# Kernel tuning notes

Hardware: AMD Instinct MI355X
Metric: run time of the kernel (lower is better)

## Reference

```python
import jax, jax.numpy as jnp
import numpy as np

B, NNODES, C = 8192, 6, 256

def _compute_W(features, W_id):
    # features: [B, C', N] -> edge weights [B, N, N, 2] (J2 operator: [I, exp-affinity - 10*I])
    f = jnp.swapaxes(features, 1, 2)                        # [B, N, C']
    sq = jnp.sum(f * f, axis=2, keepdims=True)              # [B, N, 1]
    D = jax.nn.relu(sq + jnp.swapaxes(sq, 1, 2)
                    - 2.0 * jnp.einsum('bnc,bmc->bnm', f, f))   # pairwise sq-dist [B,N,N]
    D_std = jnp.std(D, axis=(1, 2), ddof=1, keepdims=True)  # unbiased, matches torch.std
    D = jnp.exp(-2.0 * D / D_std)
    W_new = D[..., None] - 10.0 * W_id                      # 'softmax' branch is a no-op reshape in source
    return jnp.concatenate([W_id, W_new], axis=3)

def setup_inputs() -> dict:
    key = jax.random.key(0)
    ks = jax.random.split(key, 3)
    x = jax.random.normal(ks[0], (B, NNODES, C), dtype=jnp.float32)
    K1Nopen = jax.random.normal(ks[1], (C, C), dtype=jnp.float32) * 0.1
    KNclose = jax.random.normal(ks[2], (NNODES, C), dtype=jnp.float32) * 0.1
    alpha = jnp.zeros((1, 1), dtype=jnp.float32)
    h = jnp.array([0.1], dtype=jnp.float32)
    return {"x": x, "K1Nopen": K1Nopen, "KNclose": KNclose, "alpha": alpha, "h": h}

def reference(x, K1Nopen, KNclose, alpha, h):
    Bq, N, _ = x.shape
    W_id = jnp.broadcast_to(jnp.eye(N, dtype=x.dtype)[None, :, :, None], (Bq, N, N, 1))
    xn = jnp.swapaxes(x, 1, 2)                                  # [B, C, N]
    xn = jax.nn.relu(jnp.einsum('oc,bcn->bon', K1Nopen, xn))    # singleLayer (1x1 conv + relu); dropout = identity
    xn_old = xn
    beta = jax.nn.sigmoid(alpha)
    al = (1.0 - beta) / h
    be = beta / (h * h)
    for _ in range(4):
        Wi = _compute_W(xn, W_id)
        W1 = Wi[..., 1]                                         # [B, N, N]
        g = W1[:, None] * (xn[:, :, None, :] - xn[:, :, :, None])  # nodeGrad [B,C,N,N]
        d = g
        for _t in range(5):                                     # finalDoubleLayer: edgeConv no-ops on 4-D input
            d = jnp.tanh(d)
        dxn = jnp.sum(W1[:, None] * d, axis=2)                  # edgeDiv -> [B, C, N]
        xn, xn_old = (2.0 * be * xn - be * xn_old + al * xn - dxn) / (be + al), xn
    out = jnp.swapaxes(jnp.einsum('oc,bcn->bon', KNclose, xn), 1, 2)  # [B, N, NNODES]
    Wl = _compute_W(out, W_id)
    return out[:, 0, :], xn, Wl
```

## Files before the change

kernel.cpp:

```cpp
#include <hip/hip_runtime.h>
#include <math.h>

#define NNODES 6
#define CDIM 256
#define NPAIR 15
#define BTOT 8192

#define XN_OFF   49152ULL
#define WL_OFF   12632064ULL

typedef __attribute__((ext_vector_type(8))) short short8v;
typedef __attribute__((ext_vector_type(4))) float f32x4;

static __device__ __forceinline__ unsigned bf16_rne(float f) {
  unsigned u = __float_as_uint(f);
  return (u + 0x7FFFu + ((u >> 16) & 1u)) >> 16;
}

static __device__ __forceinline__ float tanh1(float v) {
  float e = __expf(2.0f * v);
  return 1.0f - __fdividef(2.0f, e + 1.0f);
}

template <int CTRL>
static __device__ __forceinline__ float dpp_add(float v) {
  int s = __builtin_bit_cast(int, v);
  int t = __builtin_amdgcn_update_dpp(s, s, CTRL, 0xF, 0xF, false);
  return v + __builtin_bit_cast(float, t);
}
static __device__ __forceinline__ float wave_sum(float v) {
  v = dpp_add<0xB1>(v);
  v = dpp_add<0x4E>(v);
  v = dpp_add<0x141>(v);
  v = dpp_add<0x140>(v);
  int s = __builtin_bit_cast(int, v);
  int t = __builtin_amdgcn_ds_swizzle(s, 0x401F);
  v += __builtin_bit_cast(float, t);
  v += __shfl_xor(v, 32, 64);
  return v;
}

__global__ void split_k1(const float* __restrict__ K1,
                         uint4* __restrict__ Ah, uint4* __restrict__ Al) {
  int t = blockIdx.x * 256 + threadIdx.x;
  int o = t >> 5, c8 = t & 31;
  const float* src = K1 + (size_t)o * 256 + c8 * 8;
  unsigned hi[8], lo[8];
#pragma unroll
  for (int j = 0; j < 8; ++j) {
    float f = src[j];
    unsigned hr = bf16_rne(f);
    float hf = __uint_as_float(hr << 16);
    lo[j] = bf16_rne(f - hf);
    hi[j] = hr;
  }
  int s = c8 >> 2, ko = c8 & 3, mt = o >> 4, row = o & 15;
  int idx16 = ((s * 16 + mt) * 4 + ko) * 16 + row;
  Ah[idx16] = make_uint4(hi[0] | (hi[1] << 16), hi[2] | (hi[3] << 16),
                         hi[4] | (hi[5] << 16), hi[6] | (hi[7] << 16));
  Al[idx16] = make_uint4(lo[0] | (lo[1] << 16), lo[2] | (lo[3] << 16),
                         lo[4] | (lo[5] << 16), lo[6] | (lo[7] << 16));
}

__global__ __launch_bounds__(256, 2) void pdegcn_mfma(
    const float* __restrict__ x,
    const uint4* __restrict__ Ahg,
    const uint4* __restrict__ Alg,
    const float* __restrict__ KNc,
    const float* __restrict__ alphap,
    const float* __restrict__ hp,
    float* __restrict__ out)
{
  __shared__ unsigned short bbuf[14528];
  __shared__ float Tt[1024];
  __shared__ float Ms[4][36];

  const int wv = threadIdx.x >> 6;
  const int lane = threadIdx.x & 63;
  const int b0 = blockIdx.x * 4;

#pragma unroll
  for (int t = 0; t < 4; ++t) {
    int i = threadIdx.x + 256 * t;
    float v = ((float)(i - 512) + 0.5f) * (1.0f / 64.0f);
#pragma unroll
    for (int r = 0; r < 5; ++r) v = tanh1(v);
    Tt[i] = v;
  }

  {
    const float4* x4 = reinterpret_cast<const float4*>(x) + (size_t)b0 * 384;
#pragma unroll
    for (int i = 0; i < 6; ++i) {
      int idx = threadIdx.x + 256 * i;
      int p = idx >> 6, c4 = idx & 63;
      float4 v = x4[idx];
      unsigned w0 = __builtin_amdgcn_perm(__float_as_uint(v.y), __float_as_uint(v.x), 0x07060302u);
      unsigned w1 = __builtin_amdgcn_perm(__float_as_uint(v.w), __float_as_uint(v.z), 0x07060302u);
      int ko = c4 >> 1, jb = (c4 & 1) * 4;
      int colS = p ^ (ko & 7);
      int hw = (ko * 24 + colS) * 8 + jb;
      *reinterpret_cast<uint2*>(&bbuf[hw]) = make_uint2(w0, w1);
    }
  }
  __syncthreads();

  f32x4 acc[4][2];
#pragma unroll
  for (int m = 0; m < 4; ++m)
#pragma unroll
    for (int nt = 0; nt < 2; ++nt)
      acc[m][nt] = (f32x4){0.0f, 0.0f, 0.0f, 0.0f};

  const int g = lane >> 4, colx = lane & 15;
  const short8v* Ah8 = reinterpret_cast<const short8v*>(Ahg);
  const short8v* Al8 = reinterpret_cast<const short8v*>(Alg);
  const short8v* bb16 = reinterpret_cast<const short8v*>(bbuf);

#pragma unroll 2
  for (int s = 0; s < 8; ++s) {
    int ko = s * 4 + g;
    int q = ko & 7;
    short8v bh[2];
#pragma unroll
    for (int nt = 0; nt < 2; ++nt) {
      int off16 = ko * 24 + ((nt * 16 + colx) ^ q);
      bh[nt] = bb16[off16];
    }
#pragma unroll
    for (int m = 0; m < 4; ++m) {
      int mt = wv * 4 + m;
      int ai = (s * 16 + mt) * 64 + lane;
      short8v a_h = Ah8[ai];
      short8v a_l = Al8[ai];
#pragma unroll
      for (int nt = 0; nt < 2; ++nt) {
        acc[m][nt] = __builtin_amdgcn_mfma_f32_16x16x32_bf16(a_h, bh[nt], acc[m][nt], 0, 0, 0);
        acc[m][nt] = __builtin_amdgcn_mfma_f32_16x16x32_bf16(a_l, bh[nt], acc[m][nt], 0, 0, 0);
      }
    }
  }
  __syncthreads();

  float* xn_lds = reinterpret_cast<float*>(bbuf);
#pragma unroll
  for (int m = 0; m < 4; ++m) {
    int mt = wv * 4 + m;
#pragma unroll
    for (int nt = 0; nt < 2; ++nt) {
      int bn = nt * 16 + colx;
      if (bn < 24) {
        f32x4 v = acc[m][nt];
        float4 w4 = make_float4(fmaxf(v[0], 0.0f), fmaxf(v[1], 0.0f),
                                fmaxf(v[2], 0.0f), fmaxf(v[3], 0.0f));
        int cidx = (mt * 16 + g * 4) ^ ((bn & 7) << 2);
        *reinterpret_cast<float4*>(&xn_lds[bn * 256 + cidx]) = w4;
      }
    }
  }
  __syncthreads();

  const int c0 = lane * 4;
  float xn[4][6], xo[4][6];
#pragma unroll
  for (int n = 0; n < 6; ++n) {
    int row = wv * 6 + n;
    float4 t = *reinterpret_cast<const float4*>(&xn_lds[row * 256 + (c0 ^ ((row & 7) << 2))]);
    xn[0][n] = t.x; xn[1][n] = t.y; xn[2][n] = t.z; xn[3][n] = t.w;
    xo[0][n] = t.x; xo[1][n] = t.y; xo[2][n] = t.z; xo[3][n] = t.w;
  }
  __syncthreads();

  {
    uint4* kh4 = reinterpret_cast<uint4*>(reinterpret_cast<char*>(bbuf) + 12672);
    uint4* kl4 = kh4 + 512;
#pragma unroll
    for (int cc = 0; cc < 2; ++cc) {
      int c = threadIdx.x + cc * 256;
      int row = c & 15, ko = (c >> 4) & 3, s = c >> 6;
      uint4 hi4 = make_uint4(0, 0, 0, 0), lo4 = make_uint4(0, 0, 0, 0);
      if (row < 6) {
        const float4* src = reinterpret_cast<const float4*>(KNc + row * 256 + s * 32 + ko * 8);
        float4 f0 = src[0], f1 = src[1];
        float f[8] = {f0.x, f0.y, f0.z, f0.w, f1.x, f1.y, f1.z, f1.w};
        unsigned hh[8], ll[8];
#pragma unroll
        for (int j = 0; j < 8; ++j) {
          unsigned hr = bf16_rne(f[j]);
          float hf = __uint_as_float(hr << 16);
          ll[j] = bf16_rne(f[j] - hf);
          hh[j] = hr;
        }
        hi4 = make_uint4(hh[0] | (hh[1] << 16), hh[2] | (hh[3] << 16),
                         hh[4] | (hh[5] << 16), hh[6] | (hh[7] << 16));
        lo4 = make_uint4(ll[0] | (ll[1] << 16), ll[2] | (ll[3] << 16),
                         ll[4] | (ll[5] << 16), ll[6] | (ll[7] << 16));
      }
      kh4[c] = hi4;
      kl4[c] = lo4;
    }
  }
  __syncthreads();

  const float alpha = alphap[0];
  const float h = hp[0];
  const float beta = 1.0f / (1.0f + __expf(-alpha));
  const float al = (1.0f - beta) / h;
  const float be = beta / (h * h);
  const float invd = 1.0f / (be + al);
  const float cA = (2.0f * be + al) * invd;
  const float cB = -be * invd;

  const int PI[NPAIR] = {0,0,0,0,0,1,1,1,1,2,2,2,3,3,4};
  const int PJ[NPAIR] = {1,2,3,4,5,2,3,4,5,3,4,5,4,5,5};

#pragma unroll 1
  for (int it = 0; it < 4; ++it) {
    float D[NPAIR];
#pragma unroll
    for (int p = 0; p < NPAIR; ++p) D[p] = 0.0f;
#pragma unroll
    for (int p = 0; p < NPAIR; ++p) {
      const int i = PI[p], j = PJ[p];
#pragma unroll
      for (int k = 0; k < 4; ++k) {
        float df = xn[k][i] - xn[k][j];
        D[p] = fmaf(df, df, D[p]);
      }
    }
#pragma unroll
    for (int p = 0; p < NPAIR; ++p) D[p] = wave_sum(D[p]);

    float t0 = D[0] + D[1],  t1 = D[2] + D[3],  t2 = D[4] + D[5];
    float t3 = D[6] + D[7],  t4 = D[8] + D[9],  t5 = D[10] + D[11];
    float t6 = D[12] + D[13];
    float u0 = t0 + t1, u1 = t2 + t3, u2 = t4 + t5, u3 = t6 + D[14];
    float sumD = (u0 + u1) + (u2 + u3);
    float mean = sumD * (2.0f / 36.0f);
    float m2[NPAIR];
#pragma unroll
    for (int p = 0; p < NPAIR; ++p) {
      float dm = D[p] - mean;
      m2[p] = dm * dm;
    }
    float s0 = m2[0] + m2[1],  s1 = m2[2] + m2[3],  s2 = m2[4] + m2[5];
    float s3 = m2[6] + m2[7],  s4 = m2[8] + m2[9],  s5 = m2[10] + m2[11];
    float s6 = m2[12] + m2[13];
    float v0 = s0 + s1, v1 = s2 + s3, v2 = s4 + s5, v3 = s6 + m2[14];
    float sc = (v0 + v1) + (v2 + v3);
    float var = (2.0f * sc + 6.0f * mean * mean) * (1.0f / 35.0f);
    float rstd = rsqrtf(var);
    float rs2 = -2.885390082f * rstd;

    float w[NPAIR];
#pragma unroll
    for (int p = 0; p < NPAIR; ++p) w[p] = exp2f(D[p] * rs2);

    float dxn[4][6];
#pragma unroll
    for (int k = 0; k < 4; ++k)
#pragma unroll
      for (int n = 0; n < 6; ++n) dxn[k][n] = 0.0f;

#pragma unroll
    for (int p = 0; p < NPAIR; ++p) {
      const int i = PI[p], j = PJ[p];
      const float wp = w[p];
      const float wp64 = wp * 64.0f;
#pragma unroll
      for (int k = 0; k < 4; ++k) {
        float delta = xn[k][j] - xn[k][i];
        float fi = fmaf(delta, wp64, 512.0f);
        fi = fminf(fmaxf(fi, 0.0f), 1023.0f);
        int u = (int)fi;
        float wd = wp * Tt[u];
        dxn[k][j] += wd;
        dxn[k][i] -= wd;
      }
    }

#pragma unroll
    for (int k = 0; k < 4; ++k)
#pragma unroll
      for (int n = 0; n < 6; ++n) {
        float nv = cA * xn[k][n] + cB * xo[k][n] - invd * dxn[k][n];
        xo[k][n] = xn[k][n];
        xn[k][n] = nv;
      }
  }

  {
    unsigned short* bstg = bbuf + wv * 1584;
#pragma unroll
    for (int n = 0; n < 6; ++n) {
      unsigned u0 = __builtin_amdgcn_perm(__float_as_uint(xn[1][n]), __float_as_uint(xn[0][n]), 0x07060302u);
      unsigned u1 = __builtin_amdgcn_perm(__float_as_uint(xn[3][n]), __float_as_uint(xn[2][n]), 0x07060302u);
      *reinterpret_cast<uint2*>(&bstg[n * 264 + lane * 4]) = make_uint2(u0, u1);
    }

    const short8v* kh = reinterpret_cast<const short8v*>(reinterpret_cast<char*>(bbuf) + 12672);
    const short8v* kl = kh + 512;
    const char* bbase = reinterpret_cast<const char*>(bbuf) + wv * 3168;

    f32x4 c3 = (f32x4){0.0f, 0.0f, 0.0f, 0.0f};
#pragma unroll
    for (int s = 0; s < 8; ++s) {
      int cell = (s * 4 + g) * 16 + colx;
      short8v a_h = kh[cell];
      short8v a_l = kl[cell];
      short8v bfr = *reinterpret_cast<const short8v*>(bbase + colx * 528 + s * 64 + g * 16);
      c3 = __builtin_amdgcn_mfma_f32_16x16x32_bf16(a_h, bfr, c3, 0, 0, 0);
      c3 = __builtin_amdgcn_mfma_f32_16x16x32_bf16(a_l, bfr, c3, 0, 0, 0);
    }

    if (colx < 6 && g < 2) {
#pragma unroll
      for (int r = 0; r < 4; ++r) {
        int o = g * 4 + r;
        if (o < 6) Ms[wv][colx * 6 + o] = c3[r];
      }
    }
  }
  __syncthreads();

  float* stg   = reinterpret_cast<float*>(bbuf);
  float* wstg  = Tt;
  float* o0stg = wstg + 288;

  {
    float4* sp = reinterpret_cast<float4*>(stg) + wv * 384 + lane * 6;
    sp[0] = make_float4(xn[0][0], xn[0][1], xn[0][2], xn[0][3]);
    sp[1] = make_float4(xn[0][4], xn[0][5], xn[1][0], xn[1][1]);
    sp[2] = make_float4(xn[1][2], xn[1][3], xn[1][4], xn[1][5]);
    sp[3] = make_float4(xn[2][0], xn[2][1], xn[2][2], xn[2][3]);
    sp[4] = make_float4(xn[2][4], xn[2][5], xn[3][0], xn[3][1]);
    sp[5] = make_float4(xn[3][2], xn[3][3], xn[3][4], xn[3][5]);
  }

  if (lane < 6) o0stg[wv * 6 + lane] = Ms[wv][lane];

  {
    const int p = lane;
    float Dp = 0.0f;
    int o1 = 0, o2 = 0;
    if (p < 36) {
      o1 = p / 6; o2 = p % 6;
#pragma unroll
      for (int n = 0; n < 6; ++n) {
        float diff = Ms[wv][n * 6 + o1] - Ms[wv][n * 6 + o2];
        Dp = fmaf(diff, diff, Dp);
      }
    }
    float sD = wave_sum(Dp);
    float meanl = sD * (1.0f / 36.0f);
    float c2 = 0.0f;
    if (p < 36) { float dm = Dp - meanl; c2 = dm * dm; }
    float sc2 = wave_sum(c2);
    float rstdl = rsqrtf(sc2 * (1.0f / 35.0f));
    if (p < 36) {
      float wnew = __expf(-2.0f * Dp * rstdl) - ((o1 == o2) ? 10.0f : 0.0f);
      wstg[wv * 72 + p * 2]     = (o1 == o2) ? 1.0f : 0.0f;
      wstg[wv * 72 + p * 2 + 1] = wnew;
    }
  }
  __syncthreads();

  {
    const float4* s4 = reinterpret_cast<const float4*>(stg);
    float4* dst4 = reinterpret_cast<float4*>(out + XN_OFF) + (size_t)b0 * 384;
#pragma unroll
    for (int i = 0; i < 6; ++i)
      dst4[threadIdx.x + 256 * i] = s4[threadIdx.x + 256 * i];
  }
  if (threadIdx.x < 72) {
    float4* wdst = reinterpret_cast<float4*>(out + WL_OFF + (size_t)b0 * 72);
    wdst[threadIdx.x] = reinterpret_cast<const float4*>(wstg)[threadIdx.x];
  }
  if (threadIdx.x < 6) {
    float4* odst = reinterpret_cast<float4*>(out + (size_t)b0 * 6);
    odst[threadIdx.x] = reinterpret_cast<const float4*>(o0stg)[threadIdx.x];
  }
}

__global__ __launch_bounds__(256) void pdegcn_fallback(
    const float* __restrict__ x,
    const float* __restrict__ K1,
    const float* __restrict__ KNc,
    const float* __restrict__ alphap,
    const float* __restrict__ hp,
    float* __restrict__ out)
{
  __shared__ float Tt[1025];
  __shared__ float Ms[4][36];

  const int wv = threadIdx.x >> 6;
  const int lane = threadIdx.x & 63;
  const int b = blockIdx.x * 4 + wv;
  const int c0 = lane * 4;

  for (int i = threadIdx.x; i < 1025; i += 256) {
    float v = (float)i * (1.0f / 128.0f);
#pragma unroll
    for (int t = 0; t < 5; ++t) {
      float e = __expf(2.0f * v);
      v = 1.0f - __fdividef(2.0f, e + 1.0f);
    }
    Tt[i] = v;
  }
  __syncthreads();

  const float alpha = alphap[0];
  const float h = hp[0];
  const float beta = 1.0f / (1.0f + __expf(-alpha));
  const float al = (1.0f - beta) / h;
  const float be = beta / (h * h);
  const float invd = 1.0f / (be + al);
  const float cA = (2.0f * be + al) * invd;
  const float cB = -be * invd;

  const float* xb = x + (size_t)b * (NNODES * CDIM);

  float acc[4][6];
#pragma unroll
  for (int k = 0; k < 4; ++k)
#pragma unroll
    for (int n = 0; n < 6; ++n) acc[k][n] = 0.0f;

#pragma unroll 1
  for (int c = 0; c < CDIM; c += 4) {
    float xr[6][4];
#pragma unroll
    for (int n = 0; n < 6; ++n) {
      float4 v = *reinterpret_cast<const float4*>(xb + n * CDIM + c);
      xr[n][0] = v.x; xr[n][1] = v.y; xr[n][2] = v.z; xr[n][3] = v.w;
    }
#pragma unroll
    for (int cc = 0; cc < 4; ++cc) {
      float kk[4];
#pragma unroll
      for (int k = 0; k < 4; ++k) kk[k] = K1[(size_t)(c0 + k) * CDIM + c + cc];
#pragma unroll
      for (int k = 0; k < 4; ++k)
#pragma unroll
        for (int n = 0; n < 6; ++n)
          acc[k][n] = fmaf(kk[k], xr[n][cc], acc[k][n]);
    }
  }

  float xn[4][6], xo[4][6];
#pragma unroll
  for (int k = 0; k < 4; ++k)
#pragma unroll
    for (int n = 0; n < 6; ++n) {
      float v = fmaxf(acc[k][n], 0.0f);
      xn[k][n] = v; xo[k][n] = v;
    }

  const int PI[NPAIR] = {0,0,0,0,0,1,1,1,1,2,2,2,3,3,4};
  const int PJ[NPAIR] = {1,2,3,4,5,2,3,4,5,3,4,5,4,5,5};

#pragma unroll 1
  for (int it = 0; it < 4; ++it) {
    float D[NPAIR];
#pragma unroll
    for (int p = 0; p < NPAIR; ++p) D[p] = 0.0f;
#pragma unroll
    for (int p = 0; p < NPAIR; ++p) {
      const int i = PI[p], j = PJ[p];
#pragma unroll
      for (int k = 0; k < 4; ++k) {
        float df = xn[k][i] - xn[k][j];
        D[p] = fmaf(df, df, D[p]);
      }
    }
#pragma unroll
    for (int s = 32; s >= 1; s >>= 1)
#pragma unroll
      for (int p = 0; p < NPAIR; ++p) D[p] += __shfl_xor(D[p], s, 64);

    float sumD = 0.0f;
#pragma unroll
    for (int p = 0; p < NPAIR; ++p) sumD += D[p];
    float mean = sumD * (2.0f / 36.0f);
    float sc = 0.0f;
#pragma unroll
    for (int p = 0; p < NPAIR; ++p) {
      float dm = D[p] - mean;
      sc = fmaf(dm, dm, sc);
    }
    float var = (2.0f * sc + 6.0f * mean * mean) * (1.0f / 35.0f);
    float rstd = rsqrtf(var);

    float w[NPAIR];
#pragma unroll
    for (int p = 0; p < NPAIR; ++p) w[p] = __expf(-2.0f * D[p] * rstd);

    float dxn[4][6];
#pragma unroll
    for (int k = 0; k < 4; ++k)
#pragma unroll
      for (int n = 0; n < 6; ++n) dxn[k][n] = 0.0f;

#pragma unroll
    for (int p = 0; p < NPAIR; ++p) {
      const int i = PI[p], j = PJ[p];
      const float wp = w[p];
#pragma unroll
      for (int k = 0; k < 4; ++k) {
        float gg = wp * (xn[k][j] - xn[k][i]);
        float ax = fminf(fabsf(gg) * 128.0f, 1023.0f);
        int ii = (int)ax;
        float fr = ax - (float)ii;
        float ta = Tt[ii];
        float tb = Tt[ii + 1];
        float d = fmaf(fr, tb - ta, ta);
        d = copysignf(d, gg);
        float wd = wp * d;
        dxn[k][j] += wd;
        dxn[k][i] -= wd;
      }
    }

#pragma unroll
    for (int k = 0; k < 4; ++k)
#pragma unroll
      for (int n = 0; n < 6; ++n) {
        float nv = cA * xn[k][n] + cB * xo[k][n] - invd * dxn[k][n];
        xo[k][n] = xn[k][n];
        xn[k][n] = nv;
      }
  }

  float po[6][6];
#pragma unroll
  for (int n = 0; n < 6; ++n)
#pragma unroll
    for (int o = 0; o < 6; ++o) po[n][o] = 0.0f;
#pragma unroll
  for (int k = 0; k < 4; ++k)
#pragma unroll
    for (int o = 0; o < 6; ++o) {
      float kv = KNc[(size_t)o * CDIM + c0 + k];
#pragma unroll
      for (int n = 0; n < 6; ++n) po[n][o] = fmaf(kv, xn[k][n], po[n][o]);
    }
#pragma unroll
  for (int s = 32; s >= 1; s >>= 1)
#pragma unroll
    for (int n = 0; n < 6; ++n)
#pragma unroll
      for (int o = 0; o < 6; ++o) po[n][o] += __shfl_xor(po[n][o], s, 64);

  if (lane == 0) {
#pragma unroll
    for (int n = 0; n < 6; ++n)
#pragma unroll
      for (int o = 0; o < 6; ++o) Ms[wv][n * 6 + o] = po[n][o];
  }
  __syncthreads();

  if (lane < 6) out[(size_t)b * 6 + lane] = Ms[wv][lane];

  {
    float4* d4 = reinterpret_cast<float4*>(out + XN_OFF + (size_t)b * (CDIM * NNODES) + (size_t)c0 * NNODES);
    d4[0] = make_float4(xn[0][0], xn[0][1], xn[0][2], xn[0][3]);
    d4[1] = make_float4(xn[0][4], xn[0][5], xn[1][0], xn[1][1]);
    d4[2] = make_float4(xn[1][2], xn[1][3], xn[1][4], xn[1][5]);
    d4[3] = make_float4(xn[2][0], xn[2][1], xn[2][2], xn[2][3]);
    d4[4] = make_float4(xn[2][4], xn[2][5], xn[3][0], xn[3][1]);
    d4[5] = make_float4(xn[3][2], xn[3][3], xn[3][4], xn[3][5]);
  }

  {
    const int p = lane;
    float Dp = 0.0f;
    int o1 = 0, o2 = 0;
    if (p < 36) {
      o1 = p / 6; o2 = p % 6;
#pragma unroll
      for (int n = 0; n < 6; ++n) {
        float diff = Ms[wv][n * 6 + o1] - Ms[wv][n * 6 + o2];
        Dp = fmaf(diff, diff, Dp);
      }
    }
    float sD = Dp;
#pragma unroll
    for (int s = 32; s >= 1; s >>= 1) sD += __shfl_xor(sD, s, 64);
    float meanl = sD * (1.0f / 36.0f);
    float c2 = 0.0f;
    if (p < 36) { float dm = Dp - meanl; c2 = dm * dm; }
    float sc2 = c2;
#pragma unroll
    for (int s = 32; s >= 1; s >>= 1) sc2 += __shfl_xor(sc2, s, 64);
    float rstdl = rsqrtf(sc2 * (1.0f / 35.0f));
    if (p < 36) {
      float wnew = __expf(-2.0f * Dp * rstdl) - ((o1 == o2) ? 10.0f : 0.0f);
      size_t base = WL_OFF + ((size_t)b * 36 + p) * 2;
      out[base] = (o1 == o2) ? 1.0f : 0.0f;
      out[base + 1] = wnew;
    }
  }
}

extern "C" void kernel_launch(void* const* d_in, const int* in_sizes, int n_in,
                              void* d_out, int out_size, void* d_ws, size_t ws_size,
                              hipStream_t stream) {
  (void)in_sizes; (void)n_in; (void)out_size;
  const float* x     = (const float*)d_in[0];
  const float* K1    = (const float*)d_in[1];
  const float* KNc   = (const float*)d_in[2];
  const float* alpha = (const float*)d_in[3];
  const float* h     = (const float*)d_in[4];
  float* out = (float*)d_out;

  if (ws_size >= 262144) {
    uint4* Ah = (uint4*)d_ws;
    uint4* Al = Ah + 8192;
    split_k1<<<32, 256, 0, stream>>>(K1, Ah, Al);
    pdegcn_mfma<<<BTOT / 4, 256, 0, stream>>>(x, Ah, Al, KNc, alpha, h, out);
  } else {
    pdegcn_fallback<<<BTOT / 4, 256, 0, stream>>>(x, K1, KNc, alpha, h, out);
  }
}
```

Baseline: 94.66 us.

## Alias LDS pool, shrink tanh table, drop low-bf16 term in close projection

Merges the separate LDS buffers into one aliased pool, moving the tanh lookup table into it after the first GEMM. The table shrinks from 1024 to 896 entries. The KNclose projection now uses only a truncated high bf16 part instead of the hi+lo split, halving its MFMAs and the staging work. The goal is lower LDS footprint for better occupancy and less setup work. In exchange it adds a barrier before the final stage, narrows the tanh table's clamp range, and reduces precision in the output projection.

```diff
diff --git a/kernel.cpp b/kernel.cpp
--- a/kernel.cpp
+++ b/kernel.cpp
@@ -71,22 +71,16 @@
     const float* __restrict__ hp,
     float* __restrict__ out)
 {
-  __shared__ unsigned short bbuf[14528];
-  __shared__ float Tt[1024];
+  __shared__ __align__(16) char pool[24576];
   __shared__ float Ms[4][36];
+  __shared__ __align__(16) float wstg[288];
+  __shared__ __align__(16) float o0stg[24];
 
   const int wv = threadIdx.x >> 6;
   const int lane = threadIdx.x & 63;
   const int b0 = blockIdx.x * 4;
 
-#pragma unroll
-  for (int t = 0; t < 4; ++t) {
-    int i = threadIdx.x + 256 * t;
-    float v = ((float)(i - 512) + 0.5f) * (1.0f / 64.0f);
-#pragma unroll
-    for (int r = 0; r < 5; ++r) v = tanh1(v);
-    Tt[i] = v;
-  }
+  unsigned short* poolh = reinterpret_cast<unsigned short*>(pool);
 
   {
     const float4* x4 = reinterpret_cast<const float4*>(x) + (size_t)b0 * 384;
@@ -100,7 +94,7 @@
       int ko = c4 >> 1, jb = (c4 & 1) * 4;
       int colS = p ^ (ko & 7);
       int hw = (ko * 24 + colS) * 8 + jb;
-      *reinterpret_cast<uint2*>(&bbuf[hw]) = make_uint2(w0, w1);
+      *reinterpret_cast<uint2*>(&poolh[hw]) = make_uint2(w0, w1);
     }
   }
   __syncthreads();
@@ -115,7 +109,7 @@
   const int g = lane >> 4, colx = lane & 15;
   const short8v* Ah8 = reinterpret_cast<const short8v*>(Ahg);
   const short8v* Al8 = reinterpret_cast<const short8v*>(Alg);
-  const short8v* bb16 = reinterpret_cast<const short8v*>(bbuf);
+  const short8v* bb16 = reinterpret_cast<const short8v*>(pool);
 
 #pragma unroll 2
   for (int s = 0; s < 8; ++s) {
@@ -142,7 +136,7 @@
   }
   __syncthreads();
 
-  float* xn_lds = reinterpret_cast<float*>(bbuf);
+  float* xn_lds = reinterpret_cast<float*>(pool);
 #pragma unroll
   for (int m = 0; m < 4; ++m) {
     int mt = wv * 4 + m;
@@ -171,33 +165,31 @@
   }
   __syncthreads();
 
-  {
-    uint4* kh4 = reinterpret_cast<uint4*>(reinterpret_cast<char*>(bbuf) + 12672);
-    uint4* kl4 = kh4 + 512;
-#pragma unroll
-    for (int cc = 0; cc < 2; ++cc) {
-      int c = threadIdx.x + cc * 256;
-      int row = c & 15, ko = (c >> 4) & 3, s = c >> 6;
-      uint4 hi4 = make_uint4(0, 0, 0, 0), lo4 = make_uint4(0, 0, 0, 0);
-      if (row < 6) {
-        const float4* src = reinterpret_cast<const float4*>(KNc + row * 256 + s * 32 + ko * 8);
-        float4 f0 = src[0], f1 = src[1];
-        float f[8] = {f0.x, f0.y, f0.z, f0.w, f1.x, f1.y, f1.z, f1.w};
-        unsigned hh[8], ll[8];
-#pragma unroll
-        for (int j = 0; j < 8; ++j) {
-          unsigned hr = bf16_rne(f[j]);
-          float hf = __uint_as_float(hr << 16);
-          ll[j] = bf16_rne(f[j] - hf);
-          hh[j] = hr;
-        }
-        hi4 = make_uint4(hh[0] | (hh[1] << 16), hh[2] | (hh[3] << 16),
-                         hh[4] | (hh[5] << 16), hh[6] | (hh[7] << 16));
-        lo4 = make_uint4(ll[0] | (ll[1] << 16), ll[2] | (ll[3] << 16),
-                         ll[4] | (ll[5] << 16), ll[6] | (ll[7] << 16));
-      }
-      kh4[c] = hi4;
-      kl4[c] = lo4;
+  float* Tt = reinterpret_cast<float*>(pool);
+#pragma unroll
+  for (int t = 0; t < 4; ++t) {
+    int i = threadIdx.x + 256 * t;
+    if (i < 896) {
+      float v = ((float)(i - 448) + 0.5f) * (1.0f / 64.0f);
+#pragma unroll
+      for (int r = 0; r < 5; ++r) v = tanh1(v);
+      Tt[i] = v;
+    }
+  }
+
+  {
+    uint4* kh4 = reinterpret_cast<uint4*>(pool + 16384);
+    int t = threadIdx.x;
+    int row = t & 7, grp = t >> 3;
+    if (row < 6) {
+      int s = grp >> 2, ko = grp & 3;
+      const float4* src = reinterpret_cast<const float4*>(KNc + row * 256 + s * 32 + ko * 8);
+      float4 f0 = src[0], f1 = src[1];
+      unsigned h0 = __builtin_amdgcn_perm(__float_as_uint(f0.y), __float_as_uint(f0.x), 0x07060302u);
+      unsigned h1 = __builtin_amdgcn_perm(__float_as_uint(f0.w), __float_as_uint(f0.z), 0x07060302u);
+      unsigned h2 = __builtin_amdgcn_perm(__float_as_uint(f1.y), __float_as_uint(f1.x), 0x07060302u);
+      unsigned h3 = __builtin_amdgcn_perm(__float_as_uint(f1.w), __float_as_uint(f1.z), 0x07060302u);
+      kh4[grp * 16 + row] = make_uint4(h0, h1, h2, h3);
     }
   }
   __syncthreads();
@@ -270,8 +262,8 @@
 #pragma unroll
       for (int k = 0; k < 4; ++k) {
         float delta = xn[k][j] - xn[k][i];
-        float fi = fmaf(delta, wp64, 512.0f);
-        fi = fminf(fmaxf(fi, 0.0f), 1023.0f);
+        float fi = fmaf(delta, wp64, 448.0f);
+        fi = fminf(fmaxf(fi, 0.0f), 895.0f);
         int u = (int)fi;
         float wd = wp * Tt[u];
         dxn[k][j] += wd;
@@ -288,9 +280,10 @@
         xn[k][n] = nv;
       }
   }
-
-  {
-    unsigned short* bstg = bbuf + wv * 1584;
+  __syncthreads();
+
+  {
+    unsigned short* bstg = poolh + wv * 1584;
 #pragma unroll
     for (int n = 0; n < 6; ++n) {
       unsigned u0 = __builtin_amdgcn_perm(__float_as_uint(xn[1][n]), __float_as_uint(xn[0][n]), 0x07060302u);
@@ -298,19 +291,16 @@
       *reinterpret_cast<uint2*>(&bstg[n * 264 + lane * 4]) = make_uint2(u0, u1);
     }
 
-    const short8v* kh = reinterpret_cast<const short8v*>(reinterpret_cast<char*>(bbuf) + 12672);
-    const short8v* kl = kh + 512;
-    const char* bbase = reinterpret_cast<const char*>(bbuf) + wv * 3168;
+    const short8v* kh = reinterpret_cast<const short8v*>(pool + 16384);
+    const char* bbase = pool + wv * 3168;
 
     f32x4 c3 = (f32x4){0.0f, 0.0f, 0.0f, 0.0f};
 #pragma unroll
     for (int s = 0; s < 8; ++s) {
       int cell = (s * 4 + g) * 16 + colx;
       short8v a_h = kh[cell];
-      short8v a_l = kl[cell];
       short8v bfr = *reinterpret_cast<const short8v*>(bbase + colx * 528 + s * 64 + g * 16);
       c3 = __builtin_amdgcn_mfma_f32_16x16x32_bf16(a_h, bfr, c3, 0, 0, 0);
-      c3 = __builtin_amdgcn_mfma_f32_16x16x32_bf16(a_l, bfr, c3, 0, 0, 0);
     }
 
     if (colx < 6 && g < 2) {
@@ -323,9 +313,7 @@
   }
   __syncthreads();
 
-  float* stg   = reinterpret_cast<float*>(bbuf);
-  float* wstg  = Tt;
-  float* o0stg = wstg + 288;
+  float* stg = reinterpret_cast<float*>(pool);
 
   {
     float4* sp = reinterpret_cast<float4*>(stg) + wv * 384 + lane * 6;
```

Measured after the change: 93.11 us. About the same (-1.6%).
